# Kernel optimization log

Measured on AMD Instinct MI355X. Metric: run time of the kernel, lower is better.

Reference implementation:

```python
import jax, jax.numpy as jnp
import numpy as np

EMB = 128
HID = 64
B = 4096
H = 200


def setup_inputs() -> dict:
    key = jax.random.key(0)
    ks = jax.random.split(key, 9)
    historical_embs = jax.random.normal(ks[0], (B, H, EMB), dtype=jnp.float32)
    candidate_emb = jax.random.normal(ks[1], (B, EMB), dtype=jnp.float32)
    mask = jax.random.randint(ks[2], (B, H), 0, 2, dtype=jnp.int32)
    # attention_net params: Linear(2*EMB -> HID), Linear(HID -> HID//2), Linear(HID//2 -> 1)
    def init_linear(k, fan_in, fan_out):
        k1, k2 = jax.random.split(k)
        bound = 1.0 / np.sqrt(fan_in)
        W = jax.random.uniform(k1, (fan_in, fan_out), jnp.float32, -bound, bound)
        b = jax.random.uniform(k2, (fan_out,), jnp.float32, -bound, bound)
        return W, b
    W1, b1 = init_linear(ks[3], 2 * EMB, HID)
    W2, b2 = init_linear(ks[4], HID, HID // 2)
    W3, b3 = init_linear(ks[5], HID // 2, 1)
    return {
        "historical_embs": historical_embs,
        "candidate_emb": candidate_emb,
        "W1": W1, "b1": b1, "W2": W2, "b2": b2, "W3": W3, "b3": b3,
        "mask": mask,
    }


def reference(historical_embs, candidate_emb, W1, b1, W2, b2, W3, b3, mask):
    # [B, H, 2*EMB] concat of history and broadcast candidate
    num_history = historical_embs.shape[1]
    cand = jnp.broadcast_to(candidate_emb[:, None, :], historical_embs.shape)
    combined = jnp.concatenate([historical_embs, cand], axis=-1)
    h = jax.nn.relu(combined @ W1 + b1)          # [B, H, HID]
    h = jax.nn.relu(h @ W2 + b2)                 # [B, H, HID//2]
    scores = (h @ W3 + b3)[..., 0]               # [B, H]
    scores = scores + (1.0 - mask.astype(scores.dtype)) * -1e9
    attention_weights = jax.nn.softmax(scores, axis=1)  # [B, H]
    aggregated = jnp.einsum('bh,bhd->bd', attention_weights, historical_embs)
    return aggregated, attention_weights
```

## Files before the change

kernel.cpp:

```cpp
#include <hip/hip_runtime.h>

#define EMB  128
#define HID  64
#define NH   200
#define BT   256
#define LDX  132
#define LDH1 68

#define WS_FRAG_BYTES 32768

typedef _Float16 half_t;
typedef half_t half2v __attribute__((ext_vector_type(2)));
typedef half_t half4v __attribute__((ext_vector_type(4)));
typedef half_t half8v __attribute__((ext_vector_type(8)));
typedef float  f32x4  __attribute__((ext_vector_type(4)));

__global__ __launch_bounds__(BT) void precomp_kernel(
    const float* __restrict__ W1, const float* __restrict__ b1,
    const float* __restrict__ W2, const float* __restrict__ cand,
    half8v* __restrict__ frag_ws, float* __restrict__ c1_ws, int nblk_c1)
{
    const int tid = threadIdx.x;
    if ((int)blockIdx.x == nblk_c1) {
        const int lane = tid & 63, wid = tid >> 6;
        const int c16 = lane & 15, quad = lane >> 4;
        half8v f[8];
        #pragma unroll
        for (int ks = 0; ks < 4; ++ks)
            #pragma unroll
            for (int j = 0; j < 8; ++j)
                f[ks][j] = (half_t)W1[(ks * 32 + quad * 8 + j) * HID + wid * 16 + c16];
        #pragma unroll
        for (int nt = 0; nt < 2; ++nt)
            #pragma unroll
            for (int ks = 0; ks < 2; ++ks)
                #pragma unroll
                for (int j = 0; j < 8; ++j)
                    f[4 + nt * 2 + ks][j] =
                        (half_t)W2[(ks * 32 + quad * 8 + j) * (HID / 2) + nt * 16 + c16];
        #pragma unroll
        for (int i = 0; i < 8; ++i) frag_ws[tid * 8 + i] = f[i];
    } else {
        __shared__ float W1b_s[EMB * HID];
        __shared__ float cand_s[4 * EMB];
        const int b0 = blockIdx.x * 4;
        for (int i = tid; i < EMB * HID; i += BT) W1b_s[i] = W1[EMB * HID + i];
        for (int i = tid; i < 4 * EMB; i += BT) cand_s[i] = cand[(size_t)b0 * EMB + i];
        __syncthreads();
        const int bl = tid >> 6, j = tid & 63;
        float acc = b1[j];
        #pragma unroll 8
        for (int k = 0; k < EMB; ++k)
            acc = fmaf(cand_s[bl * EMB + k], W1b_s[k * HID + j], acc);
        c1_ws[(size_t)(b0 + bl) * HID + j] = acc;
    }
}

__global__ __launch_bounds__(BT, 2) void attn_agg_kernel(
    const float* __restrict__ hist,
    const half8v* __restrict__ frag_ws,
    const float* __restrict__ c1_ws,
    const float* __restrict__ b2,
    const float* __restrict__ W3,
    const int*   __restrict__ mask,
    float* __restrict__ out_agg,
    float* __restrict__ out_attn)
{
    __shared__ __align__(16) half_t X_s[NH * LDX];
    __shared__ __align__(16) half_t H1_s[NH * LDH1];
    __shared__ float c1_s[HID];
    __shared__ float attn_s[NH];

    const int b    = blockIdx.x;
    const int tid  = threadIdx.x;
    const int lane = tid & 63;
    const int wid  = tid >> 6;
    const int c16  = lane & 15;
    const int quad = lane >> 4;

    const float* hb = hist + (size_t)b * (NH * EMB);

    const half8v* fw = frag_ws + tid * 8;
    half8v w1f[4];
    w1f[0] = fw[0]; w1f[1] = fw[1]; w1f[2] = fw[2]; w1f[3] = fw[3];
    half8v w2f[2][2];
    w2f[0][0] = fw[4]; w2f[0][1] = fw[5]; w2f[1][0] = fw[6]; w2f[1][1] = fw[7];

    const float w3a  = W3[c16];
    const float w3b  = W3[16 + c16];
    const float bb2a = b2[c16];
    const float bb2b = b2[16 + c16];

    if (tid < HID) c1_s[tid] = c1_ws[(size_t)b * HID + tid];

    {
        const float4* src = (const float4*)hb;
        #pragma unroll 5
        for (int t = 0; t < 25; ++t) {
            int i = t * BT + tid;
            int h = i >> 5, c4 = i & 31;
            float4 v = src[i];
            half2v p0 = {(half_t)v.x, (half_t)v.y};
            half2v p1 = {(half_t)v.z, (half_t)v.w};
            *(half2v*)&X_s[h * LDX + c4 * 4]     = p0;
            *(half2v*)&X_s[h * LDX + c4 * 4 + 2] = p1;
        }
    }
    __syncthreads();

    {
        const float c1v = c1_s[wid * 16 + c16];
        for (int t = 0; t < 13; ++t) {
            const int m0 = (t < 12) ? t * 16 : 184;
            const int row = m0 + c16;
            f32x4 acc = {0.f, 0.f, 0.f, 0.f};
            #pragma unroll
            for (int ks = 0; ks < 4; ++ks) {
                const half_t* ap = &X_s[row * LDX + ks * 32 + quad * 8];
                half4v alo = *(const half4v*)ap;
                half4v ahi = *(const half4v*)(ap + 4);
                half8v a = __builtin_shufflevector(alo, ahi, 0, 1, 2, 3, 4, 5, 6, 7);
                acc = __builtin_amdgcn_mfma_f32_16x16x32_f16(a, w1f[ks], acc, 0, 0, 0);
            }
            #pragma unroll
            for (int i = 0; i < 4; ++i) {
                int r = m0 + 4 * quad + i;
                float hv = fmaxf(acc[i] + c1v, 0.f);
                H1_s[r * LDH1 + wid * 16 + c16] = (half_t)hv;
            }
        }
    }
    __syncthreads();

    for (int t = wid; t < 13; t += 4) {
        const int m0 = (t < 12) ? t * 16 : 184;
        const int row = m0 + c16;
        f32x4 acc0 = {0.f, 0.f, 0.f, 0.f};
        f32x4 acc1 = {0.f, 0.f, 0.f, 0.f};
        #pragma unroll
        for (int ks = 0; ks < 2; ++ks) {
            const half_t* ap = &H1_s[row * LDH1 + ks * 32 + quad * 8];
            half4v alo = *(const half4v*)ap;
            half4v ahi = *(const half4v*)(ap + 4);
            half8v a = __builtin_shufflevector(alo, ahi, 0, 1, 2, 3, 4, 5, 6, 7);
            acc0 = __builtin_amdgcn_mfma_f32_16x16x32_f16(a, w2f[0][ks], acc0, 0, 0, 0);
            acc1 = __builtin_amdgcn_mfma_f32_16x16x32_f16(a, w2f[1][ks], acc1, 0, 0, 0);
        }
        float sp[4];
        #pragma unroll
        for (int i = 0; i < 4; ++i)
            sp[i] = fmaxf(acc0[i] + bb2a, 0.f) * w3a + fmaxf(acc1[i] + bb2b, 0.f) * w3b;
        #pragma unroll
        for (int m = 1; m < 16; m <<= 1)
            #pragma unroll
            for (int i = 0; i < 4; ++i)
                sp[i] += __shfl_xor(sp[i], m, 64);
        if (c16 == 0) {
            const int lo = (t == 12) ? 192 : m0;
            #pragma unroll
            for (int i = 0; i < 4; ++i) {
                int r = m0 + 4 * quad + i;
                if (r >= lo) attn_s[r] = sp[i];
            }
        }
    }
    __syncthreads();

    if (tid < 64) {
        const int* mb = mask + (size_t)b * NH;
        float s0 = attn_s[tid]       + (1.f - (float)mb[tid])       * -1e9f;
        float s1 = attn_s[64 + tid]  + (1.f - (float)mb[64 + tid])  * -1e9f;
        float s2 = attn_s[128 + tid] + (1.f - (float)mb[128 + tid]) * -1e9f;
        float s3 = (tid < 8) ? attn_s[192 + tid] + (1.f - (float)mb[192 + tid]) * -1e9f : -1e30f;
        float m = fmaxf(fmaxf(s0, s1), fmaxf(s2, s3));
        #pragma unroll
        for (int off = 32; off; off >>= 1) m = fmaxf(m, __shfl_xor(m, off, 64));
        float e0 = __expf(s0 - m);
        float e1 = __expf(s1 - m);
        float e2 = __expf(s2 - m);
        float e3 = (tid < 8) ? __expf(s3 - m) : 0.f;
        float sum = e0 + e1 + e2 + e3;
        #pragma unroll
        for (int off = 32; off; off >>= 1) sum += __shfl_xor(sum, off, 64);
        float inv = 1.f / sum;
        e0 *= inv; e1 *= inv; e2 *= inv; e3 *= inv;
        attn_s[tid] = e0; attn_s[64 + tid] = e1; attn_s[128 + tid] = e2;
        if (tid < 8) attn_s[192 + tid] = e3;
        float* oa = out_attn + (size_t)b * NH;
        oa[tid] = e0; oa[64 + tid] = e1; oa[128 + tid] = e2;
        if (tid < 8) oa[192 + tid] = e3;
    }
    __syncthreads();

    {
        int c = tid & 63;
        int g = wid;
        float2 acc = make_float2(0.f, 0.f);
        for (int h = g * 50; h < g * 50 + 50; ++h) {
            float w = attn_s[h];
            half2v v = *(const half2v*)&X_s[h * LDX + c * 2];
            acc.x = fmaf(w, (float)v[0], acc.x);
            acc.y = fmaf(w, (float)v[1], acc.y);
        }
        __syncthreads();
        float2* red = (float2*)X_s;
        red[g * 64 + c] = acc;
        __syncthreads();
        if (tid < 64) {
            float2 r0 = red[tid], r1 = red[64 + tid], r2 = red[128 + tid], r3 = red[192 + tid];
            float2 o = make_float2(r0.x + r1.x + r2.x + r3.x,
                                   r0.y + r1.y + r2.y + r3.y);
            *(float2*)&out_agg[(size_t)b * EMB + tid * 2] = o;
        }
    }
}

extern "C" void kernel_launch(void* const* d_in, const int* in_sizes, int n_in,
                              void* d_out, int out_size, void* d_ws, size_t ws_size,
                              hipStream_t stream) {
    const float* hist = (const float*)d_in[0];
    const float* cand = (const float*)d_in[1];
    const float* W1   = (const float*)d_in[2];
    const float* b1   = (const float*)d_in[3];
    const float* W2   = (const float*)d_in[4];
    const float* b2   = (const float*)d_in[5];
    const float* W3   = (const float*)d_in[6];
    const int*   mask = (const int*)d_in[8];

    const int B = in_sizes[0] / (NH * EMB);
    float* out_agg  = (float*)d_out;
    float* out_attn = out_agg + (size_t)B * EMB;

    half8v* frag_ws = (half8v*)d_ws;
    float*  c1_ws   = (float*)((char*)d_ws + WS_FRAG_BYTES);

    const int nblk_c1 = B / 4;
    precomp_kernel<<<nblk_c1 + 1, BT, 0, stream>>>(W1, b1, W2, cand, frag_ws, c1_ws, nblk_c1);
    attn_agg_kernel<<<B, BT, 0, stream>>>(hist, frag_ws, c1_ws, b2, W3, mask,
                                          out_agg, out_attn);
}
```

Measured before the change: 575.1 us.

## Stream history directly from global into MFMA operands, dropping the shared-memory X tile

The attention kernel no longer stages the fp32 history, converted to fp16, in a large shared-memory tile. Each wave now loads its MFMA A operands straight from global memory and converts them in registers, and the weighted aggregation re-reads the history from global (likely served by cache). This cuts shared memory per block to allow 4 blocks per CU instead of 2, trading LDS traffic and a barrier for extra global and cache traffic. The weight fragment layout is also reorganised so each wave reads only the fragments it needs.

```diff
diff --git a/kernel.cpp b/kernel.cpp
--- a/kernel.cpp
+++ b/kernel.cpp
@@ -4,7 +4,6 @@
 #define HID  64
 #define NH   200
 #define BT   256
-#define LDX  132
 #define LDH1 68
 
 #define WS_FRAG_BYTES 32768
@@ -14,6 +13,13 @@
 typedef half_t half4v __attribute__((ext_vector_type(4)));
 typedef half_t half8v __attribute__((ext_vector_type(8)));
 typedef float  f32x4  __attribute__((ext_vector_type(4)));
+
+static __device__ __forceinline__ half8v cvt8(float4 a, float4 b) {
+    half8v r;
+    r[0] = (half_t)a.x; r[1] = (half_t)a.y; r[2] = (half_t)a.z; r[3] = (half_t)a.w;
+    r[4] = (half_t)b.x; r[5] = (half_t)b.y; r[6] = (half_t)b.z; r[7] = (half_t)b.w;
+    return r;
+}
 
 __global__ __launch_bounds__(BT) void precomp_kernel(
     const float* __restrict__ W1, const float* __restrict__ b1,
@@ -24,28 +30,38 @@
     if ((int)blockIdx.x == nblk_c1) {
         const int lane = tid & 63, wid = tid >> 6;
         const int c16 = lane & 15, quad = lane >> 4;
-        half8v f[8];
-        #pragma unroll
-        for (int ks = 0; ks < 4; ++ks)
+        #pragma unroll
+        for (int ks = 0; ks < 4; ++ks) {
+            half8v f;
             #pragma unroll
             for (int j = 0; j < 8; ++j)
-                f[ks][j] = (half_t)W1[(ks * 32 + quad * 8 + j) * HID + wid * 16 + c16];
-        #pragma unroll
-        for (int nt = 0; nt < 2; ++nt)
-            #pragma unroll
-            for (int ks = 0; ks < 2; ++ks)
+                f[j] = (half_t)W1[(ks * 32 + quad * 8 + j) * HID + wid * 16 + c16];
+            frag_ws[(wid * 4 + ks) * 64 + lane] = f;
+        }
+        if (wid == 0) {
+            #pragma unroll
+            for (int nt = 0; nt < 2; ++nt)
                 #pragma unroll
-                for (int j = 0; j < 8; ++j)
-                    f[4 + nt * 2 + ks][j] =
-                        (half_t)W2[(ks * 32 + quad * 8 + j) * (HID / 2) + nt * 16 + c16];
-        #pragma unroll
-        for (int i = 0; i < 8; ++i) frag_ws[tid * 8 + i] = f[i];
+                for (int ks = 0; ks < 2; ++ks) {
+                    half8v f;
+                    #pragma unroll
+                    for (int j = 0; j < 8; ++j)
+                        f[j] = (half_t)W2[(ks * 32 + quad * 8 + j) * (HID / 2) + nt * 16 + c16];
+                    frag_ws[1024 + (nt * 2 + ks) * 64 + lane] = f;
+                }
+        }
     } else {
         __shared__ float W1b_s[EMB * HID];
         __shared__ float cand_s[4 * EMB];
         const int b0 = blockIdx.x * 4;
-        for (int i = tid; i < EMB * HID; i += BT) W1b_s[i] = W1[EMB * HID + i];
-        for (int i = tid; i < 4 * EMB; i += BT) cand_s[i] = cand[(size_t)b0 * EMB + i];
+        {
+            const float4* src = (const float4*)(W1 + EMB * HID);
+            float4* dst = (float4*)W1b_s;
+            for (int i = tid; i < EMB * HID / 4; i += BT) dst[i] = src[i];
+            const float4* csrc = (const float4*)(cand + (size_t)b0 * EMB);
+            float4* cdst = (float4*)cand_s;
+            for (int i = tid; i < EMB; i += BT) cdst[i] = csrc[i];
+        }
         __syncthreads();
         const int bl = tid >> 6, j = tid & 63;
         float acc = b1[j];
@@ -56,7 +72,7 @@
     }
 }
 
-__global__ __launch_bounds__(BT, 2) void attn_agg_kernel(
+__global__ __launch_bounds__(BT, 4) void attn_agg_kernel(
     const float* __restrict__ hist,
     const half8v* __restrict__ frag_ws,
     const float* __restrict__ c1_ws,
@@ -66,10 +82,9 @@
     float* __restrict__ out_agg,
     float* __restrict__ out_attn)
 {
-    __shared__ __align__(16) half_t X_s[NH * LDX];
     __shared__ __align__(16) half_t H1_s[NH * LDH1];
-    __shared__ float c1_s[HID];
     __shared__ float attn_s[NH];
+    __shared__ float2 red_s[BT];
 
     const int b    = blockIdx.x;
     const int tid  = threadIdx.x;
@@ -80,57 +95,46 @@
 
     const float* hb = hist + (size_t)b * (NH * EMB);
 
-    const half8v* fw = frag_ws + tid * 8;
     half8v w1f[4];
-    w1f[0] = fw[0]; w1f[1] = fw[1]; w1f[2] = fw[2]; w1f[3] = fw[3];
+    #pragma unroll
+    for (int ks = 0; ks < 4; ++ks)
+        w1f[ks] = frag_ws[(wid * 4 + ks) * 64 + lane];
+
+    const float c1v = c1_ws[(size_t)b * HID + wid * 16 + c16];
+
+    for (int t = 0; t < 13; ++t) {
+        const int m0 = (t < 12) ? t * 16 : 184;
+        const float* rp = hb + (m0 + c16) * EMB + quad * 8;
+        float4 x0a = *(const float4*)(rp);
+        float4 x0b = *(const float4*)(rp + 4);
+        float4 x1a = *(const float4*)(rp + 32);
+        float4 x1b = *(const float4*)(rp + 36);
+        float4 x2a = *(const float4*)(rp + 64);
+        float4 x2b = *(const float4*)(rp + 68);
+        float4 x3a = *(const float4*)(rp + 96);
+        float4 x3b = *(const float4*)(rp + 100);
+        f32x4 acc = {0.f, 0.f, 0.f, 0.f};
+        acc = __builtin_amdgcn_mfma_f32_16x16x32_f16(cvt8(x0a, x0b), w1f[0], acc, 0, 0, 0);
+        acc = __builtin_amdgcn_mfma_f32_16x16x32_f16(cvt8(x1a, x1b), w1f[1], acc, 0, 0, 0);
+        acc = __builtin_amdgcn_mfma_f32_16x16x32_f16(cvt8(x2a, x2b), w1f[2], acc, 0, 0, 0);
+        acc = __builtin_amdgcn_mfma_f32_16x16x32_f16(cvt8(x3a, x3b), w1f[3], acc, 0, 0, 0);
+        #pragma unroll
+        for (int i = 0; i < 4; ++i) {
+            int r = m0 + 4 * quad + i;
+            H1_s[r * LDH1 + wid * 16 + c16] = (half_t)fmaxf(acc[i] + c1v, 0.f);
+        }
+    }
+    __syncthreads();
+
     half8v w2f[2][2];
-    w2f[0][0] = fw[4]; w2f[0][1] = fw[5]; w2f[1][0] = fw[6]; w2f[1][1] = fw[7];
-
+    w2f[0][0] = frag_ws[1024 + 0 * 64 + lane];
+    w2f[0][1] = frag_ws[1024 + 1 * 64 + lane];
+    w2f[1][0] = frag_ws[1024 + 2 * 64 + lane];
+    w2f[1][1] = frag_ws[1024 + 3 * 64 + lane];
     const float w3a  = W3[c16];
     const float w3b  = W3[16 + c16];
     const float bb2a = b2[c16];
     const float bb2b = b2[16 + c16];
-
-    if (tid < HID) c1_s[tid] = c1_ws[(size_t)b * HID + tid];
-
-    {
-        const float4* src = (const float4*)hb;
-        #pragma unroll 5
-        for (int t = 0; t < 25; ++t) {
-            int i = t * BT + tid;
-            int h = i >> 5, c4 = i & 31;
-            float4 v = src[i];
-            half2v p0 = {(half_t)v.x, (half_t)v.y};
-            half2v p1 = {(half_t)v.z, (half_t)v.w};
-            *(half2v*)&X_s[h * LDX + c4 * 4]     = p0;
-            *(half2v*)&X_s[h * LDX + c4 * 4 + 2] = p1;
-        }
-    }
-    __syncthreads();
-
-    {
-        const float c1v = c1_s[wid * 16 + c16];
-        for (int t = 0; t < 13; ++t) {
-            const int m0 = (t < 12) ? t * 16 : 184;
-            const int row = m0 + c16;
-            f32x4 acc = {0.f, 0.f, 0.f, 0.f};
-            #pragma unroll
-            for (int ks = 0; ks < 4; ++ks) {
-                const half_t* ap = &X_s[row * LDX + ks * 32 + quad * 8];
-                half4v alo = *(const half4v*)ap;
-                half4v ahi = *(const half4v*)(ap + 4);
-                half8v a = __builtin_shufflevector(alo, ahi, 0, 1, 2, 3, 4, 5, 6, 7);
-                acc = __builtin_amdgcn_mfma_f32_16x16x32_f16(a, w1f[ks], acc, 0, 0, 0);
-            }
-            #pragma unroll
-            for (int i = 0; i < 4; ++i) {
-                int r = m0 + 4 * quad + i;
-                float hv = fmaxf(acc[i] + c1v, 0.f);
-                H1_s[r * LDH1 + wid * 16 + c16] = (half_t)hv;
-            }
-        }
-    }
-    __syncthreads();
 
     for (int t = wid; t < 13; t += 4) {
         const int m0 = (t < 12) ? t * 16 : 184;
@@ -193,21 +197,21 @@
     __syncthreads();
 
     {
-        int c = tid & 63;
-        int g = wid;
+        const int c = tid & 63;
+        const int g = wid;
         float2 acc = make_float2(0.f, 0.f);
-        for (int h = g * 50; h < g * 50 + 50; ++h) {
-            float w = attn_s[h];
-            half2v v = *(const half2v*)&X_s[h * LDX + c * 2];
-            acc.x = fmaf(w, (float)v[0], acc.x);
-            acc.y = fmaf(w, (float)v[1], acc.y);
-        }
-        __syncthreads();
-        float2* red = (float2*)X_s;
-        red[g * 64 + c] = acc;
+        const float* xp = hb + g * 50 * EMB + 2 * c;
+        #pragma unroll 5
+        for (int h = 0; h < 50; ++h) {
+            float w = attn_s[g * 50 + h];
+            float2 v = *(const float2*)(xp + (size_t)h * EMB);
+            acc.x = fmaf(w, v.x, acc.x);
+            acc.y = fmaf(w, v.y, acc.y);
+        }
+        red_s[tid] = acc;
         __syncthreads();
         if (tid < 64) {
-            float2 r0 = red[tid], r1 = red[64 + tid], r2 = red[128 + tid], r3 = red[192 + tid];
+            float2 r0 = red_s[tid], r1 = red_s[64 + tid], r2 = red_s[128 + tid], r3 = red_s[192 + tid];
             float2 o = make_float2(r0.x + r1.x + r2.x + r3.x,
                                    r0.y + r1.y + r2.y + r3.y);
             *(float2*)&out_agg[(size_t)b * EMB + tid * 2] = o;
@@ -227,15 +231,18 @@
     const float* W3   = (const float*)d_in[6];
     const int*   mask = (const int*)d_in[8];
 
-    const int B = in_sizes[0] / (NH * EMB);
+    const int B = in_sizes[0] / (NH * EMB * 4);
+    const int Brows = in_sizes[0] / (NH * EMB);
+    (void)B;
+
     float* out_agg  = (float*)d_out;
-    float* out_attn = out_agg + (size_t)B * EMB;
+    float* out_attn = out_agg + (size_t)Brows * EMB;
 
     half8v* frag_ws = (half8v*)d_ws;
     float*  c1_ws   = (float*)((char*)d_ws + WS_FRAG_BYTES);
 
-    const int nblk_c1 = B / 4;
+    const int nblk_c1 = Brows / 4;
     precomp_kernel<<<nblk_c1 + 1, BT, 0, stream>>>(W1, b1, W2, cand, frag_ws, c1_ws, nblk_c1);
-    attn_agg_kernel<<<B, BT, 0, stream>>>(hist, frag_ws, c1_ws, b2, W3, mask,
-                                          out_agg, out_attn);
-}
+    attn_agg_kernel<<<Brows, BT, 0, stream>>>(hist, frag_ws, c1_ws, b2, W3, mask,
+                                              out_agg, out_attn);
+}
```

Result: slower. 661.8 us (+15.1%).
